# Kernel optimization log

Hardware: AMD Instinct MI355X
Metric: run time of the kernel (lower is better)

Reference implementation:

```python
import jax, jax.numpy as jnp
import numpy as np

B, D, S = 16384, 2048, 512      # batch, input_dim, sideinfo_dim
E, H1, H2 = 8, 1024, 512        # subexpert_num, subexpert_unit
EPS = 1e-5                       # BatchNorm eps (torch default)


def setup_inputs() -> dict:
    key = jax.random.key(0)
    ks = jax.random.split(key, 16)
    inp = {
        "input": jax.random.normal(ks[0], (B, D), jnp.float32),
        "sideinfo": jax.random.normal(ks[1], (B, S), jnp.float32),
        # expert layer 1: Linear(D->H1) per expert, batched over E
        "W1": jax.random.normal(ks[2], (E, D, H1), jnp.float32) / np.sqrt(D),
        "b1": jax.random.normal(ks[3], (E, H1), jnp.float32) * 0.01,
        "gamma1": 1.0 + 0.01 * jax.random.normal(ks[4], (E, H1), jnp.float32),
        "beta1": jax.random.normal(ks[5], (E, H1), jnp.float32) * 0.01,
        "mean1": jax.random.normal(ks[6], (E, H1), jnp.float32) * 0.01,
        "var1": jax.random.uniform(ks[7], (E, H1), jnp.float32, 0.5, 1.5),
        # expert layer 2: Linear(H1->H2) per expert
        "W2": jax.random.normal(ks[8], (E, H1, H2), jnp.float32) / np.sqrt(H1),
        "b2": jax.random.normal(ks[9], (E, H2), jnp.float32) * 0.01,
        "gamma2": 1.0 + 0.01 * jax.random.normal(ks[10], (E, H2), jnp.float32),
        "beta2": jax.random.normal(ks[11], (E, H2), jnp.float32) * 0.01,
        "mean2": jax.random.normal(ks[12], (E, H2), jnp.float32) * 0.01,
        "var2": jax.random.uniform(ks[13], (E, H2), jnp.float32, 0.5, 1.5),
        # gate: Linear(S->E) + softmax
        "Wg": jax.random.normal(ks[14], (S, E), jnp.float32) / np.sqrt(S),
        "bg": jax.random.normal(ks[15], (E,), jnp.float32) * 0.01,
    }
    return inp


def _bn(x, gamma, beta, mean, var):
    # eval-mode BatchNorm1d with per-expert running stats; x: [B,E,H]
    return (x - mean) * (gamma * jax.lax.rsqrt(var + EPS)) + beta


def reference(input, sideinfo, W1, b1, gamma1, beta1, mean1, var1,
              W2, b2, gamma2, beta2, mean2, var2, Wg, bg):
    # all E expert MLPs as two batched GEMMs (dropout is identity in eval)
    h = jnp.einsum('bd,edh->beh', input, W1) + b1            # [B,E,H1]
    h = jax.nn.relu(_bn(h, gamma1, beta1, mean1, var1))
    o = jnp.einsum('beh,eho->beo', h, W2) + b2               # [B,E,H2]
    o = jax.nn.relu(_bn(o, gamma2, beta2, mean2, var2))
    gate = jax.nn.softmax(sideinfo @ Wg + bg, axis=1)        # [B,E]
    return jnp.einsum('beo,be->bo', o, gate)                 # [B,H2]
```

## Files before the change

### kernel.cpp

```cpp
#include <hip/hip_runtime.h>
#include <hip/hip_bf16.h>

static constexpr int B_  = 16384;
static constexpr int D_  = 2048;
static constexpr int S_  = 512;
static constexpr int E_  = 8;
static constexpr int H1_ = 1024;
static constexpr int H2_ = 512;
static constexpr float EPS_ = 1e-5f;

typedef __bf16 bf16x8 __attribute__((ext_vector_type(8)));
typedef float  f32x4  __attribute__((ext_vector_type(4)));

static __device__ __forceinline__ unsigned short f2bf(float f) {
    unsigned u = __float_as_uint(f);
    unsigned r = (u + 0x7fffu + ((u >> 16) & 1u)) >> 16;
    return (unsigned short)r;
}


__global__ void cvt_bf16_kernel(const float* __restrict__ in, ushort* __restrict__ out, long n) {
    long i = ((long)blockIdx.x * blockDim.x + threadIdx.x) * 4;
    long stride = (long)gridDim.x * blockDim.x * 4;
    for (; i < n; i += stride) {
        float4 v = *(const float4*)(in + i);
        ushort4 o;
        o.x = f2bf(v.x); o.y = f2bf(v.y); o.z = f2bf(v.z); o.w = f2bf(v.w);
        *(ushort4*)(out + i) = o;
    }
}

__global__ void transpose_cvt_kernel(const float* __restrict__ in, ushort* __restrict__ out,
                                     int R, int C) {
    __shared__ float t[64][65];
    int nbr = R >> 6, nbc = C >> 6;
    int bid = blockIdx.x;
    int e = bid / (nbr * nbc);
    int rem = bid % (nbr * nbc);
    int br = (rem / nbc) << 6, bc = (rem % nbc) << 6;
    const float* ip = in + (size_t)e * R * C;
    ushort* op = out + (size_t)e * R * C;
    int tcol = (threadIdx.x & 15) * 4;
    int trow = threadIdx.x >> 4;
#pragma unroll
    for (int p = 0; p < 4; p++) {
        int r = trow + p * 16;
        float4 v = *(const float4*)(ip + (size_t)(br + r) * C + bc + tcol);
        t[r][tcol + 0] = v.x; t[r][tcol + 1] = v.y; t[r][tcol + 2] = v.z; t[r][tcol + 3] = v.w;
    }
    __syncthreads();
#pragma unroll
    for (int p = 0; p < 4; p++) {
        int c = trow + p * 16;
        ushort4 o;
        o.x = f2bf(t[tcol + 0][c]);
        o.y = f2bf(t[tcol + 1][c]);
        o.z = f2bf(t[tcol + 2][c]);
        o.w = f2bf(t[tcol + 3][c]);
        *(ushort4*)(op + (size_t)(bc + c) * R + br + tcol) = o;
    }
}

__global__ void fold_bn_kernel(const float* __restrict__ gamma, const float* __restrict__ beta,
                               const float* __restrict__ mean, const float* __restrict__ var,
                               const float* __restrict__ bias,
                               float* __restrict__ Sv, float* __restrict__ Tv, int n) {
    int i = blockIdx.x * 256 + threadIdx.x;
    if (i < n) {
        float s = gamma[i] * rsqrtf(var[i] + EPS_);
        Sv[i] = s;
        Tv[i] = (bias[i] - mean[i]) * s + beta[i];
    }
}

__global__ void gate_kernel(const float* __restrict__ side, const float* __restrict__ Wg,
                            const float* __restrict__ bg, float* __restrict__ gate) {
    int wid = threadIdx.x >> 6, lane = threadIdx.x & 63;
    int b = blockIdx.x * 4 + wid;
    const float* sp = side + (size_t)b * S_ + lane * 8;
    float4 v0 = *(const float4*)sp;
    float4 v1 = *(const float4*)(sp + 4);
    float sv[8] = {v0.x, v0.y, v0.z, v0.w, v1.x, v1.y, v1.z, v1.w};
    float acc[E_] = {0,0,0,0,0,0,0,0};
    const float* wrow = Wg + (size_t)(lane * 8) * E_;
#pragma unroll
    for (int j = 0; j < 8; j++) {
        float4 w0 = *(const float4*)(wrow + j * E_);
        float4 w1 = *(const float4*)(wrow + j * E_ + 4);
        acc[0] += sv[j] * w0.x; acc[1] += sv[j] * w0.y;
        acc[2] += sv[j] * w0.z; acc[3] += sv[j] * w0.w;
        acc[4] += sv[j] * w1.x; acc[5] += sv[j] * w1.y;
        acc[6] += sv[j] * w1.z; acc[7] += sv[j] * w1.w;
    }
#pragma unroll
    for (int off = 32; off; off >>= 1)
#pragma unroll
        for (int e = 0; e < E_; e++) acc[e] += __shfl_xor(acc[e], off, 64);
    float m = -1e30f;
#pragma unroll
    for (int e = 0; e < E_; e++) { acc[e] += bg[e]; m = fmaxf(m, acc[e]); }
    float s = 0.f;
#pragma unroll
    for (int e = 0; e < E_; e++) { acc[e] = __expf(acc[e] - m); s += acc[e]; }
    float inv = 1.f / s;
    if (lane < E_) gate[(size_t)b * E_ + lane] = acc[lane] * inv;
}


__device__ __forceinline__ void g2lds16(const void* g, void* l) {
    __builtin_amdgcn_global_load_lds((const __attribute__((address_space(1))) unsigned int*)g,
                                     (__attribute__((address_space(3))) unsigned int*)l,
                                     16, 0, 0);
}

#define BAR()      asm volatile("s_barrier" ::: "memory")
#define WAITVM(n)  asm volatile("s_waitcnt vmcnt(" #n ")" ::: "memory")
#define MFMA(a,b,c) __builtin_amdgcn_mfma_f32_16x16x32_bf16((a),(b),(c),0,0,0)


template<int EPI>
__global__ __launch_bounds__(512, 2)
void gemm8(const ushort* __restrict__ A, const ushort* __restrict__ Bt, long aBatch,
           const float* __restrict__ Sv, const float* __restrict__ Tv,
           ushort* __restrict__ hout, float* __restrict__ outp, const float* __restrict__ gate,
           int M, int N, int K, int tilesN, int tilesM)
{
    extern __shared__ char smem[];

    const int NT  = K >> 6;
    const int tpe = tilesM * tilesN;

    const int nwg = gridDim.x, per = nwg >> 3;
    const int b0  = blockIdx.x;
    const int bid = (b0 & 7) * per + (b0 >> 3);

    const int e   = bid / tpe;
    const int rem = bid % tpe;
    const int tm  = rem / tilesN, tn = rem % tilesN;

    const char* aBase = (const char*)(A + (size_t)e * aBatch + (size_t)tm * 256 * K);
    const char* bBase = (const char*)(Bt + (size_t)e * N * K + (size_t)tn * 256 * K);
    const size_t rowB = (size_t)K * 2;
    const size_t half2 = 64 * rowB;
    const size_t half1 = 128 * rowB;

    const int tid = threadIdx.x, w = tid >> 6, lane = tid & 63;
    const int wm = w >> 2, wn = w & 3;

    const int srow = tid >> 3;
    const int scol_sw = ((tid & 7) * 16) ^ ((srow & 7) << 4);
    const int ldsW = w * 1024;

    const int lr = lane & 15;
    const int cks0 = ((lane >> 4) * 16) ^ ((lane & 7) << 4);
    const int cks1 = (64 + (lane >> 4) * 16) ^ ((lane & 7) << 4);
    const char* rdA0 = smem + 65536 + (wm * 128 + lr) * 128 + cks0;
    const char* rdA1 = smem + 65536 + (wm * 128 + lr) * 128 + cks1;
    const char* rdB0 = smem + (wn * 64 + lr) * 128 + cks0;
    const char* rdB1 = smem + (wn * 64 + lr) * 128 + cks1;

#define STG(gp, ldsoff) do { \
        g2lds16((gp), smem + (ldsoff)); \
        g2lds16((gp) + half2, smem + (ldsoff) + 8192); } while (0)

    const char* ga = aBase + (size_t)srow * rowB + scol_sw;
    const char* gb = bBase + (size_t)srow * rowB + scol_sw;

    f32x4 acc[8][4] = {};
    bf16x8 aC[4], aN[4], bC[4], bN[4];

    STG(ga,         65536 + 0 + 0     + ldsW);
    STG(ga + half1, 65536 + 0 + 16384 + ldsW);
    STG(gb,         0     + 0 + 0     + ldsW);
    STG(gb + half1, 0     + 0 + 16384 + ldsW);
    WAITVM(0);
    BAR();

#pragma unroll
    for (int mf = 0; mf < 4; ++mf) aC[mf] = *(const bf16x8*)(rdA0 + mf * 2048);
#pragma unroll
    for (int nf = 0; nf < 4; ++nf) bC[nf] = *(const bf16x8*)(rdB0 + nf * 2048);

    const char* spA0 = ga + 128;
    const char* spA1 = ga + half1 + 128;
    const char* spB0 = gb + 128;
    const char* spB1 = gb + half1 + 128;

#pragma unroll 2
    for (int t = 0; t < NT; ++t) {
        const int bi   = t & 1;
        const int oR   = bi * 32768;
        const int oRN  = (bi ^ 1) * 32768;
        const int oSA  = 65536 + (bi ^ 1) * 32768;
        const int oSB  = (bi ^ 1) * 32768;
        const bool more = (t < NT - 1);

#pragma unroll
        for (int mf = 0; mf < 4; ++mf) aN[mf] = *(const bf16x8*)(rdA0 + oR + (4 + mf) * 2048);
        if (more) {
            STG(spA0, oSA + 0 + ldsW);
            STG(spA1, oSA + 16384 + ldsW);
        }
        __builtin_amdgcn_s_setprio(1);
#pragma unroll
        for (int mf = 0; mf < 4; ++mf)
#pragma unroll
            for (int nf = 0; nf < 4; ++nf)
                acc[mf][nf] = MFMA(aC[mf], bC[nf], acc[mf][nf]);
        __builtin_amdgcn_s_setprio(0);

#pragma unroll
        for (int mf = 0; mf < 4; ++mf) aC[mf] = *(const bf16x8*)(rdA1 + oR + mf * 2048);
#pragma unroll
        for (int nf = 0; nf < 4; ++nf) bN[nf] = *(const bf16x8*)(rdB1 + oR + nf * 2048);
        if (more) STG(spB0, oSB + 0 + ldsW);
        __builtin_amdgcn_s_setprio(1);
#pragma unroll
        for (int mf = 0; mf < 4; ++mf)
#pragma unroll
            for (int nf = 0; nf < 4; ++nf)
                acc[4 + mf][nf] = MFMA(aN[mf], bC[nf], acc[4 + mf][nf]);
        __builtin_amdgcn_s_setprio(0);

#pragma unroll
        for (int mf = 0; mf < 4; ++mf) aN[mf] = *(const bf16x8*)(rdA1 + oR + (4 + mf) * 2048);
        if (more) STG(spB1, oSB + 16384 + ldsW);
        __builtin_amdgcn_s_setprio(1);
#pragma unroll
        for (int mf = 0; mf < 4; ++mf)
#pragma unroll
            for (int nf = 0; nf < 4; ++nf)
                acc[mf][nf] = MFMA(aC[mf], bN[nf], acc[mf][nf]);
        __builtin_amdgcn_s_setprio(0);

        __builtin_amdgcn_s_setprio(1);
#pragma unroll
        for (int mf = 0; mf < 4; ++mf)
#pragma unroll
            for (int nf = 0; nf < 4; ++nf)
                acc[4 + mf][nf] = MFMA(aN[mf], bN[nf], acc[4 + mf][nf]);
        __builtin_amdgcn_s_setprio(0);

        if (more) {
            WAITVM(0);
            BAR();
#pragma unroll
            for (int mf = 0; mf < 4; ++mf) aC[mf] = *(const bf16x8*)(rdA0 + oRN + mf * 2048);
#pragma unroll
            for (int nf = 0; nf < 4; ++nf) bC[nf] = *(const bf16x8*)(rdB0 + oRN + nf * 2048);
        }

        spA0 += 128; spA1 += 128; spB0 += 128; spB1 += 128;
    }

    const int rbase = tm * 256 + wm * 128 + (lane >> 4) * 4;
    const int cbase = tn * 256 + wn * 64 + lr;
    if (EPI == 1) {
#pragma unroll
        for (int nf = 0; nf < 4; ++nf) {
            const int col = cbase + nf * 16;
            const float s = Sv[e * N + col];
            const float tt = Tv[e * N + col];
#pragma unroll
            for (int mf = 0; mf < 8; ++mf) {
                const int row0 = rbase + mf * 16;
                f32x4 v = acc[mf][nf];
#pragma unroll
                for (int r = 0; r < 4; ++r) {
                    float x = v[r] * s + tt;
                    x = x > 0.f ? x : 0.f;
                    hout[((size_t)e * M + row0 + r) * N + col] = f2bf(x);
                }
            }
        }
    }
#undef STG
}


__global__ __launch_bounds__(512, 2)
void gemm2e(const ushort* __restrict__ H, const ushort* __restrict__ W2T,
            const float* __restrict__ Sv, const float* __restrict__ Tv,
            const float* __restrict__ gate, float* __restrict__ outp)
{
    extern __shared__ char smem[];

    const int b0 = blockIdx.x;
    const int bid = (b0 & 7) * 32 + (b0 >> 3);
    const int tm = bid >> 1, tn = bid & 1;

    const size_t rowB  = (size_t)H1_ * 2;
    const size_t strAE = (size_t)B_ * H1_ * 2;
    const size_t strBE = (size_t)H2_ * H1_ * 2;
    const size_t half2 = 64 * rowB;
    const size_t halfB = 128 * rowB;

    const int tid = threadIdx.x, w = tid >> 6, lane = tid & 63;
    const int wm = w >> 2, wn = w & 3;

    const int srow = tid >> 3;
    const int scol_sw = ((tid & 7) * 16) ^ ((srow & 7) << 4);
    const int ldsW = w * 1024;

    const int lr = lane & 15;
    const int cks0 = ((lane >> 4) * 16) ^ ((lane & 7) << 4);
    const int cks1 = (64 + (lane >> 4) * 16) ^ ((lane & 7) << 4);
    const char* rdA0 = smem + 65536 + (wm * 64 + lr) * 128 + cks0;
    const char* rdA1 = smem + 65536 + (wm * 64 + lr) * 128 + cks1;
    const char* rdB0 = smem + (wn * 64 + lr) * 128 + cks0;
    const char* rdB1 = smem + (wn * 64 + lr) * 128 + cks1;

    const char* ga = (const char*)H + (size_t)tm * 128 * rowB + (size_t)srow * rowB + scol_sw;
    const char* gb = (const char*)W2T + (size_t)tn * 256 * rowB + (size_t)srow * rowB + scol_sw;

#define STG2(gp, ldsoff) do { \
        g2lds16((gp), smem + (ldsoff)); \
        g2lds16((gp) + half2, smem + (ldsoff) + 8192); } while (0)

    f32x4 acc[4][4] = {};
    f32x4 oacc[4][4] = {};
    bf16x8 a0[4], a1[4], bb0[4], bb1[4];

    g2lds16(ga,               smem + 65536 + 0     + 0    + ldsW);
    g2lds16(ga + half2,       smem + 65536 + 0     + 8192 + ldsW);
    STG2(gb,                  0     + 0     + ldsW);
    STG2(gb + halfB,          0     + 16384 + ldsW);
    g2lds16(ga + 128,         smem + 65536 + 16384 + 0    + ldsW);
    g2lds16(ga + half2 + 128, smem + 65536 + 16384 + 8192 + ldsW);
    STG2(gb + 128,            32768 + 0     + ldsW);
    WAITVM(4);
    BAR();

    const int rbase = tm * 128 + wm * 64 + (lane >> 4) * 4;
    const int cbase = tn * 256 + wn * 64 + lr;

    for (int t = 0; t < 128; ++t) {
        const int bi  = t & 1;
        const int oA  = bi * 16384;
        const int oB  = bi * 32768;

        const int t1 = t + 1, t2 = t + 2;
        const char* gB1 = gb + (size_t)(t1 >> 4) * strBE + (t1 & 15) * 128;
        const char* gA2 = ga + (size_t)(t2 >> 4) * strAE + (t2 & 15) * 128;
        const char* gB2 = gb + (size_t)(t2 >> 4) * strBE + (t2 & 15) * 128;
        const int oA2 = 65536 + ((t2 & 1) * 16384);
        const int oB1x = (t1 & 1) * 32768;
        const int oB2 = (t2 & 1) * 32768;

#pragma unroll
        for (int mf = 0; mf < 4; ++mf) a0[mf] = *(const bf16x8*)(rdA0 + oA + mf * 2048);
#pragma unroll
        for (int nf = 0; nf < 4; ++nf) bb0[nf] = *(const bf16x8*)(rdB0 + oB + nf * 2048);
        if (t1 < 128) STG2(gB1 + halfB, oB1x + 16384 + ldsW);
        BAR();
        __builtin_amdgcn_s_setprio(1);
#pragma unroll
        for (int mf = 0; mf < 4; ++mf) {
            acc[mf][0] = MFMA(a0[mf], bb0[0], acc[mf][0]);
            acc[mf][1] = MFMA(a0[mf], bb0[1], acc[mf][1]);
        }
        __builtin_amdgcn_s_setprio(0);
        BAR();
#pragma unroll
        for (int mf = 0; mf < 4; ++mf) a1[mf] = *(const bf16x8*)(rdA1 + oA + mf * 2048);
        if (t2 < 128) {
            g2lds16(gA2, smem + oA2 + 0 + ldsW);
        }
        BAR();
        __builtin_amdgcn_s_setprio(1);
#pragma unroll
        for (int mf = 0; mf < 4; ++mf) {
            acc[mf][2] = MFMA(a0[mf], bb0[2], acc[mf][2]);
            acc[mf][3] = MFMA(a0[mf], bb0[3], acc[mf][3]);
        }
        __builtin_amdgcn_s_setprio(0);
        BAR();
#pragma unroll
        for (int nf = 0; nf < 4; ++nf) bb1[nf] = *(const bf16x8*)(rdB1 + oB + nf * 2048);
        if (t2 < 128) {
            g2lds16(gA2 + half2, smem + oA2 + 8192 + ldsW);
        }
        BAR();
        __builtin_amdgcn_s_setprio(1);
#pragma unroll
        for (int mf = 0; mf < 4; ++mf) {
            acc[mf][0] = MFMA(a1[mf], bb1[0], acc[mf][0]);
            acc[mf][1] = MFMA(a1[mf], bb1[1], acc[mf][1]);
        }
        __builtin_amdgcn_s_setprio(0);
        BAR();
        if (t2 < 128) STG2(gB2, oB2 + 0 + ldsW);
        BAR();
        __builtin_amdgcn_s_setprio(1);
#pragma unroll
        for (int mf = 0; mf < 4; ++mf) {
            acc[mf][2] = MFMA(a1[mf], bb1[2], acc[mf][2]);
            acc[mf][3] = MFMA(a1[mf], bb1[3], acc[mf][3]);
        }
        __builtin_amdgcn_s_setprio(0);
        if (t < 126)       { WAITVM(4); }
        else if (t == 126) { WAITVM(0); }
        BAR();

        if ((t & 15) == 15) {
            const int e = t >> 4;
            float sc[4], tc[4];
#pragma unroll
            for (int nf = 0; nf < 4; ++nf) {
                sc[nf] = Sv[e * H2_ + cbase + nf * 16];
                tc[nf] = Tv[e * H2_ + cbase + nf * 16];
            }
#pragma unroll
            for (int mf = 0; mf < 4; ++mf) {
#pragma unroll
                for (int r = 0; r < 4; ++r) {
                    const int row = rbase + mf * 16 + r;
                    const float g = gate[(size_t)row * E_ + e];
#pragma unroll
                    for (int nf = 0; nf < 4; ++nf) {
                        float x = acc[mf][nf][r] * sc[nf] + tc[nf];
                        x = x > 0.f ? x : 0.f;
                        oacc[mf][nf][r] += g * x;
                    }
                }
            }
#pragma unroll
            for (int mf = 0; mf < 4; ++mf)
#pragma unroll
                for (int nf = 0; nf < 4; ++nf)
                    acc[mf][nf] = (f32x4){0.f, 0.f, 0.f, 0.f};
        }
    }

#pragma unroll
    for (int mf = 0; mf < 4; ++mf) {
#pragma unroll
        for (int r = 0; r < 4; ++r) {
            const int row = rbase + mf * 16 + r;
#pragma unroll
            for (int nf = 0; nf < 4; ++nf)
                outp[(size_t)row * H2_ + cbase + nf * 16] = oacc[mf][nf][r];
        }
    }
#undef STG2
}


extern "C" void kernel_launch(void* const* d_in, const int* in_sizes, int n_in,
                              void* d_out, int out_size, void* d_ws, size_t ws_size,
                              hipStream_t stream) {
    (void)in_sizes; (void)n_in; (void)out_size; (void)ws_size;

    const float* input    = (const float*)d_in[0];
    const float* sideinfo = (const float*)d_in[1];
    const float* W1   = (const float*)d_in[2];
    const float* b1   = (const float*)d_in[3];
    const float* g1   = (const float*)d_in[4];
    const float* be1  = (const float*)d_in[5];
    const float* m1   = (const float*)d_in[6];
    const float* v1   = (const float*)d_in[7];
    const float* W2   = (const float*)d_in[8];
    const float* b2   = (const float*)d_in[9];
    const float* g2   = (const float*)d_in[10];
    const float* be2  = (const float*)d_in[11];
    const float* m2   = (const float*)d_in[12];
    const float* v2   = (const float*)d_in[13];
    const float* Wg   = (const float*)d_in[14];
    const float* bg   = (const float*)d_in[15];

    char* w = (char*)d_ws;
    size_t off = 0;
    auto carve = [&](size_t bytes) {
        void* p = w + off;
        off += (bytes + 255) & ~(size_t)255;
        return p;
    };
    ushort* Abf  = (ushort*)carve((size_t)B_ * D_ * 2);
    ushort* W1T  = (ushort*)carve((size_t)E_ * H1_ * D_ * 2);
    ushort* W2T  = (ushort*)carve((size_t)E_ * H2_ * H1_ * 2);
    ushort* hbuf = (ushort*)carve((size_t)E_ * B_ * H1_ * 2);
    float*  S1   = (float*)carve((size_t)E_ * H1_ * 4);
    float*  T1   = (float*)carve((size_t)E_ * H1_ * 4);
    float*  S2   = (float*)carve((size_t)E_ * H2_ * 4);
    float*  T2   = (float*)carve((size_t)E_ * H2_ * 4);
    float*  gatep = (float*)carve((size_t)B_ * E_ * 4);

    float* outp = (float*)d_out;

    hipFuncSetAttribute(reinterpret_cast<const void*>(&gemm8<1>),
                        hipFuncAttributeMaxDynamicSharedMemorySize, 131072);
    hipFuncSetAttribute(reinterpret_cast<const void*>(&gemm2e),
                        hipFuncAttributeMaxDynamicSharedMemorySize, 98304);

    cvt_bf16_kernel<<<4096, 256, 0, stream>>>(input, Abf, (long)B_ * D_);
    transpose_cvt_kernel<<<E_ * (D_ / 64) * (H1_ / 64), 256, 0, stream>>>(W1, W1T, D_, H1_);
    transpose_cvt_kernel<<<E_ * (H1_ / 64) * (H2_ / 64), 256, 0, stream>>>(W2, W2T, H1_, H2_);
    fold_bn_kernel<<<(E_ * H1_ + 255) / 256, 256, 0, stream>>>(g1, be1, m1, v1, b1, S1, T1, E_ * H1_);
    fold_bn_kernel<<<(E_ * H2_ + 255) / 256, 256, 0, stream>>>(g2, be2, m2, v2, b2, S2, T2, E_ * H2_);
    gate_kernel<<<B_ / 4, 256, 0, stream>>>(sideinfo, Wg, bg, gatep);

    gemm8<1><<<E_ * (B_ / 256) * (H1_ / 256), 512, 131072, stream>>>(
        Abf, W1T, 0L, S1, T1, hbuf, nullptr, nullptr, B_, H1_, D_, H1_ / 256, B_ / 256);

    gemm2e<<<(B_ / 128) * (H2_ / 256), 512, 98304, stream>>>(
        hbuf, W2T, S2, T2, gatep, outp);
}
```

Baseline: 745.4 us.

## Restructure second GEMM main loop into double-buffered pipeline with one barrier

Rewrites the second-layer GEMM inner loop. The old version prefetched two steps ahead and split each step into four MFMA phases separated by eight barriers. The new version keeps a simple double buffer: it prefetches the next K-tile while computing the current one, runs each half-K chunk as one 16-MFMA block, and synchronises once per step with a full vmcnt wait and a barrier. This removes most barrier and phase-split overhead, but shortens the prefetch distance to one step, so global-load latency may show more.

```diff
diff --git a/kernel.cpp b/kernel.cpp
--- a/kernel.cpp
+++ b/kernel.cpp
@@ -313,94 +313,78 @@
     const char* ga = (const char*)H + (size_t)tm * 128 * rowB + (size_t)srow * rowB + scol_sw;
     const char* gb = (const char*)W2T + (size_t)tn * 256 * rowB + (size_t)srow * rowB + scol_sw;
 
-#define STG2(gp, ldsoff) do { \
-        g2lds16((gp), smem + (ldsoff)); \
-        g2lds16((gp) + half2, smem + (ldsoff) + 8192); } while (0)
-
     f32x4 acc[4][4] = {};
     f32x4 oacc[4][4] = {};
-    bf16x8 a0[4], a1[4], bb0[4], bb1[4];
-
-    g2lds16(ga,               smem + 65536 + 0     + 0    + ldsW);
-    g2lds16(ga + half2,       smem + 65536 + 0     + 8192 + ldsW);
-    STG2(gb,                  0     + 0     + ldsW);
-    STG2(gb + halfB,          0     + 16384 + ldsW);
-    g2lds16(ga + 128,         smem + 65536 + 16384 + 0    + ldsW);
-    g2lds16(ga + half2 + 128, smem + 65536 + 16384 + 8192 + ldsW);
-    STG2(gb + 128,            32768 + 0     + ldsW);
-    WAITVM(4);
+    bf16x8 a0[4], a1[4], b0v[4], b1v[4];
+
+    g2lds16(ga,                 smem + 65536 + 0     + ldsW);
+    g2lds16(ga + half2,         smem + 65536 + 8192  + ldsW);
+    g2lds16(gb,                 smem + 0     + ldsW);
+    g2lds16(gb + half2,         smem + 8192  + ldsW);
+    g2lds16(gb + halfB,         smem + 16384 + ldsW);
+    g2lds16(gb + halfB + half2, smem + 24576 + ldsW);
+    WAITVM(0);
     BAR();
+
+#pragma unroll
+    for (int mf = 0; mf < 4; ++mf) a0[mf] = *(const bf16x8*)(rdA0 + mf * 2048);
+#pragma unroll
+    for (int nf = 0; nf < 4; ++nf) b0v[nf] = *(const bf16x8*)(rdB0 + nf * 2048);
 
     const int rbase = tm * 128 + wm * 64 + (lane >> 4) * 4;
     const int cbase = tn * 256 + wn * 64 + lr;
 
+#pragma unroll 2
     for (int t = 0; t < 128; ++t) {
-        const int bi  = t & 1;
-        const int oA  = bi * 16384;
-        const int oB  = bi * 32768;
-
-        const int t1 = t + 1, t2 = t + 2;
+        const int bi   = t & 1;
+        const int oA   = bi * 16384;
+        const int oB   = bi * 32768;
+        const int oAn  = (bi ^ 1) * 16384;
+        const int oBn  = (bi ^ 1) * 32768;
+        const bool more = (t < 127);
+
+        const int t1 = t + 1;
+        const char* gA1 = ga + (size_t)(t1 >> 4) * strAE + (t1 & 15) * 128;
         const char* gB1 = gb + (size_t)(t1 >> 4) * strBE + (t1 & 15) * 128;
-        const char* gA2 = ga + (size_t)(t2 >> 4) * strAE + (t2 & 15) * 128;
-        const char* gB2 = gb + (size_t)(t2 >> 4) * strBE + (t2 & 15) * 128;
-        const int oA2 = 65536 + ((t2 & 1) * 16384);
-        const int oB1x = (t1 & 1) * 32768;
-        const int oB2 = (t2 & 1) * 32768;
-
-#pragma unroll
-        for (int mf = 0; mf < 4; ++mf) a0[mf] = *(const bf16x8*)(rdA0 + oA + mf * 2048);
-#pragma unroll
-        for (int nf = 0; nf < 4; ++nf) bb0[nf] = *(const bf16x8*)(rdB0 + oB + nf * 2048);
-        if (t1 < 128) STG2(gB1 + halfB, oB1x + 16384 + ldsW);
-        BAR();
-        __builtin_amdgcn_s_setprio(1);
-#pragma unroll
-        for (int mf = 0; mf < 4; ++mf) {
-            acc[mf][0] = MFMA(a0[mf], bb0[0], acc[mf][0]);
-            acc[mf][1] = MFMA(a0[mf], bb0[1], acc[mf][1]);
-        }
-        __builtin_amdgcn_s_setprio(0);
-        BAR();
+
 #pragma unroll
         for (int mf = 0; mf < 4; ++mf) a1[mf] = *(const bf16x8*)(rdA1 + oA + mf * 2048);
-        if (t2 < 128) {
-            g2lds16(gA2, smem + oA2 + 0 + ldsW);
-        }
-        BAR();
-        __builtin_amdgcn_s_setprio(1);
-#pragma unroll
-        for (int mf = 0; mf < 4; ++mf) {
-            acc[mf][2] = MFMA(a0[mf], bb0[2], acc[mf][2]);
-            acc[mf][3] = MFMA(a0[mf], bb0[3], acc[mf][3]);
-        }
-        __builtin_amdgcn_s_setprio(0);
-        BAR();
-#pragma unroll
-        for (int nf = 0; nf < 4; ++nf) bb1[nf] = *(const bf16x8*)(rdB1 + oB + nf * 2048);
-        if (t2 < 128) {
-            g2lds16(gA2 + half2, smem + oA2 + 8192 + ldsW);
-        }
-        BAR();
-        __builtin_amdgcn_s_setprio(1);
-#pragma unroll
-        for (int mf = 0; mf < 4; ++mf) {
-            acc[mf][0] = MFMA(a1[mf], bb1[0], acc[mf][0]);
-            acc[mf][1] = MFMA(a1[mf], bb1[1], acc[mf][1]);
-        }
-        __builtin_amdgcn_s_setprio(0);
-        BAR();
-        if (t2 < 128) STG2(gB2, oB2 + 0 + ldsW);
-        BAR();
-        __builtin_amdgcn_s_setprio(1);
-#pragma unroll
-        for (int mf = 0; mf < 4; ++mf) {
-            acc[mf][2] = MFMA(a1[mf], bb1[2], acc[mf][2]);
-            acc[mf][3] = MFMA(a1[mf], bb1[3], acc[mf][3]);
-        }
-        __builtin_amdgcn_s_setprio(0);
-        if (t < 126)       { WAITVM(4); }
-        else if (t == 126) { WAITVM(0); }
-        BAR();
+#pragma unroll
+        for (int nf = 0; nf < 4; ++nf) b1v[nf] = *(const bf16x8*)(rdB1 + oB + nf * 2048);
+        if (more) {
+            g2lds16(gA1,         smem + 65536 + oAn + 0    + ldsW);
+            g2lds16(gA1 + half2, smem + 65536 + oAn + 8192 + ldsW);
+            g2lds16(gB1,         smem + oBn + 0    + ldsW);
+            g2lds16(gB1 + half2, smem + oBn + 8192 + ldsW);
+        }
+        __builtin_amdgcn_s_setprio(1);
+#pragma unroll
+        for (int mf = 0; mf < 4; ++mf)
+#pragma unroll
+            for (int nf = 0; nf < 4; ++nf)
+                acc[mf][nf] = MFMA(a0[mf], b0v[nf], acc[mf][nf]);
+        __builtin_amdgcn_s_setprio(0);
+
+        if (more) {
+            g2lds16(gB1 + halfB,         smem + oBn + 16384 + ldsW);
+            g2lds16(gB1 + halfB + half2, smem + oBn + 24576 + ldsW);
+        }
+        __builtin_amdgcn_s_setprio(1);
+#pragma unroll
+        for (int mf = 0; mf < 4; ++mf)
+#pragma unroll
+            for (int nf = 0; nf < 4; ++nf)
+                acc[mf][nf] = MFMA(a1[mf], b1v[nf], acc[mf][nf]);
+        __builtin_amdgcn_s_setprio(0);
+
+        if (more) {
+            WAITVM(0);
+            BAR();
+#pragma unroll
+            for (int mf = 0; mf < 4; ++mf) a0[mf] = *(const bf16x8*)(rdA0 + oAn + mf * 2048);
+#pragma unroll
+            for (int nf = 0; nf < 4; ++nf) b0v[nf] = *(const bf16x8*)(rdB0 + oBn + nf * 2048);
+        }
 
         if ((t & 15) == 15) {
             const int e = t >> 4;
@@ -442,7 +426,6 @@
                 outp[(size_t)row * H2_ + cbase + nf * 16] = oacc[mf][nf][r];
         }
     }
-#undef STG2
 }
 
 
```

After: 803.2 us. 1.08x slower.
